# Kernel tuning notes

Hardware: AMD Instinct MI355X
Metric: run time of the kernel (lower is better)

## Reference

```python
import jax, jax.numpy as jnp
import numpy as np

NUM_RANGES = 700
K = 250
IN_DIM = 7      # 1 power + 3 elevation embed + 3 azimuth embed
HID = 32        # Q/K hidden dim
NUM_LAYERS = 2
SCALE = 1.0 / (HID ** 0.5)


def setup_inputs() -> dict:
    key = jax.random.key(0)
    ks = jax.random.split(key, 12)
    N = NUM_RANGES * K
    inp = {
        "power_vals": jax.random.normal(ks[0], (N, 1), dtype=jnp.float32),
        "ele_indices": jax.random.randint(ks[1], (N,), 0, 37),
        "azi_indices": jax.random.randint(ks[2], (N,), 0, 107),
        # learned parameters
        "ele_emb": jax.random.normal(ks[3], (37, 3), dtype=jnp.float32),
        "azi_emb": jax.random.normal(ks[4], (107, 3), dtype=jnp.float32),
        # per-layer Q/K/V linear params, stacked over layers
        "Wq": jax.random.normal(ks[5], (NUM_LAYERS, IN_DIM, HID), dtype=jnp.float32) * 0.2,
        "bq": jax.random.normal(ks[6], (NUM_LAYERS, HID), dtype=jnp.float32) * 0.02,
        "Wk": jax.random.normal(ks[7], (NUM_LAYERS, IN_DIM, HID), dtype=jnp.float32) * 0.2,
        "bk": jax.random.normal(ks[8], (NUM_LAYERS, HID), dtype=jnp.float32) * 0.02,
        "Wv": jax.random.normal(ks[9], (NUM_LAYERS, IN_DIM, 1), dtype=jnp.float32) * 0.2,
        "bv": jax.random.normal(ks[10], (NUM_LAYERS, 1), dtype=jnp.float32) * 0.02,
    }
    return inp


def reference(power_vals, ele_indices, azi_indices, ele_emb, azi_emb, Wq, bq, Wk, bk, Wv, bv):
    # x: [R, K, 1]
    x = power_vals.reshape(NUM_RANGES, K, -1)
    # embedding lookups: [R, K, 3]
    e = ele_emb[ele_indices.reshape(NUM_RANGES, K)].astype(jnp.float32)
    a = azi_emb[azi_indices.reshape(NUM_RANGES, K)].astype(jnp.float32)
    for i in range(NUM_LAYERS):
        h = jnp.concatenate([x, e, a], axis=-1)           # [R, K, 7]
        q = h @ Wq[i] + bq[i]                             # [R, K, 32]
        k = h @ Wk[i] + bk[i]                             # [R, K, 32]
        v = h @ Wv[i] + bv[i]                             # [R, K, 1]
        scores = jnp.einsum("rqd,rkd->rqk", q, k) * SCALE  # [R, K, K]
        probs = jax.nn.softmax(scores, axis=-1)
        x = jnp.einsum("rqk,rkd->rqd", probs, v)          # [R, K, 1]
    return x.reshape(NUM_RANGES * K, 1)
```

## Files before the change

### kernel.cpp

```cpp
#include <hip/hip_runtime.h>
#include <hip/hip_fp16.h>

#define NR 700
#define KK 250
#define HID 32

typedef unsigned int uint32;
typedef _Float16 f16x8 __attribute__((ext_vector_type(8)));
typedef float f32x4 __attribute__((ext_vector_type(4)));
typedef _Float16 hpair __attribute__((ext_vector_type(2)));

#if __has_builtin(__builtin_amdgcn_exp2f)
#define EXP2F(x) __builtin_amdgcn_exp2f(x)
#else
#define EXP2F(x) exp2f(x)
#endif

__device__ __forceinline__ uint32 packh2(float lo, float hi) {
    hpair p; p.x = (_Float16)lo; p.y = (_Float16)hi;
    return __builtin_bit_cast(uint32, p);
}
__device__ __forceinline__ f16x8 u4f16(uint4 u) { return __builtin_bit_cast(f16x8, u); }

__device__ __forceinline__ void compute_weights(
    int wt, int l,
    const float* __restrict__ Wq, const float* __restrict__ bq,
    const float* __restrict__ Wk,
    const float* __restrict__ Wv, const float* __restrict__ bv,
    float (*Msh)[7], float* wsh, float* wvsh, float SC2Q)
{
    const float* wq = Wq + l * 7 * HID;
    const float* wk = Wk + l * 7 * HID;
    if (wt < 49) {
        int c = wt / 7, cp = wt % 7;
        float s = 0.f;
        #pragma unroll 8
        for (int d = 0; d < HID; ++d) s = fmaf(wq[c * HID + d], wk[cp * HID + d], s);
        Msh[c][cp] = s * SC2Q;
    } else if (wt < 56) {
        int cp = wt - 49;
        float s = 0.f;
        #pragma unroll 8
        for (int d = 0; d < HID; ++d) s = fmaf(bq[l * HID + d], wk[cp * HID + d], s);
        wsh[cp] = s * SC2Q;
    } else if (wt < 63) {
        wvsh[wt - 56] = Wv[l * 7 + (wt - 56)];
    } else if (wt == 63) {
        wvsh[7] = bv[l];
    }
}

__global__ __launch_bounds__(512, 6) void mlra_kernel(
    const float* __restrict__ power,
    const int*   __restrict__ ele_idx,
    const int*   __restrict__ azi_idx,
    const float* __restrict__ ele_emb,
    const float* __restrict__ azi_emb,
    const float* __restrict__ Wq,
    const float* __restrict__ bq,
    const float* __restrict__ Wk,
    const float* __restrict__ bk,
    const float* __restrict__ Wv,
    const float* __restrict__ bv,
    float* __restrict__ out)
{
    __shared__ uint4 hh[256];
    __shared__ uint4 tt[256];
    __shared__ float vsh[256];
    __shared__ float Msh[2][7][7];
    __shared__ float wsh[2][7];
    __shared__ float wvsh[2][8];

    const int r    = blockIdx.x;
    const int tid  = threadIdx.x;
    const int lane = tid & 63;
    const int wid  = tid >> 6;
    const int col  = lane & 15;
    const int grp  = lane >> 4;

    const float SC2Q = 0.17677669529663687f * 1.4426950408889634f * 0.25f;

    if (tid < 256) {
        float hv[7];
        if (tid < KK) {
            int g = r * KK + tid;
            hv[0] = power[g];
            int ei = ele_idx[g];
            int ai = azi_idx[g];
            hv[1] = ele_emb[ei * 3 + 0];
            hv[2] = ele_emb[ei * 3 + 1];
            hv[3] = ele_emb[ei * 3 + 2];
            hv[4] = azi_emb[ai * 3 + 0];
            hv[5] = azi_emb[ai * 3 + 1];
            hv[6] = azi_emb[ai * 3 + 2];
        } else {
            #pragma unroll
            for (int c = 0; c < 7; ++c) hv[c] = 0.f;
        }
        uint4 u;
        u.x = packh2(hv[0], hv[1]);
        u.y = packh2(hv[2], hv[3]);
        u.z = packh2(hv[4], hv[5]);
        u.w = packh2(hv[6], 0.f);
        hh[tid] = u;
        vsh[tid] = 0.f;
    } else if (tid < 384) {
        int l = (tid - 256) >> 6;
        compute_weights(tid & 63, l, Wq, bq, Wk, Wv, bv, Msh[l], wsh[l], wvsh[l], SC2Q);
    }
    __syncthreads();

    const int n0 = 2 * wid;
    const int n1 = 2 * wid + 1;
    const f32x4 cz = {0.f, 0.f, 0.f, 0.f};

    float x0 = 0.f, x1 = 0.f;

    for (int l = 0; l < 2; ++l) {
        if (tid < 256) {
            uint4 u = hh[tid];
            hpair pa = __builtin_bit_cast(hpair, u.x);
            hpair pb = __builtin_bit_cast(hpair, u.y);
            hpair pc = __builtin_bit_cast(hpair, u.z);
            hpair pd = __builtin_bit_cast(hpair, u.w);
            float hv[7] = {(float)pa.x, (float)pa.y, (float)pb.x, (float)pb.y,
                           (float)pc.x, (float)pc.y, (float)pd.x};
            float tv[7];
            #pragma unroll
            for (int cp = 0; cp < 7; ++cp) {
                float s = wsh[l][cp];
                #pragma unroll
                for (int c = 0; c < 7; ++c) s = fmaf(hv[c], Msh[l][c][cp], s);
                tv[cp] = s;
            }
            float v = wvsh[l][7];
            #pragma unroll
            for (int c = 0; c < 7; ++c) v = fmaf(hv[c], wvsh[l][c], v);
            uint4 t4;
            t4.x = packh2(tv[0], tv[1]);
            t4.y = packh2(tv[2], tv[3]);
            t4.z = packh2(tv[4], tv[5]);
            t4.w = packh2(tv[6], 0.f);
            tt[tid] = t4;
            vsh[tid] = (tid < KK) ? v : 0.f;
        }
        __syncthreads();

        f16x8 bt0 = u4f16(tt[n0 * 16 + col]);
        f16x8 bt1 = u4f16(tt[n1 * 16 + col]);

        float ss0 = 0.f, oo0 = 0.f, ss1 = 0.f, oo1 = 0.f;
        #pragma unroll 2
        for (int jt = 0; jt < 16; ++jt) {
            f16x8 ah = u4f16(hh[jt * 16 + col]);
            f32x4 vv = *reinterpret_cast<const f32x4*>(&vsh[jt * 16 + grp * 4]);
            f32x4 c0 = __builtin_amdgcn_mfma_f32_16x16x32_f16(ah, bt0, cz, 0, 0, 0);
            f32x4 c1 = __builtin_amdgcn_mfma_f32_16x16x32_f16(ah, bt1, cz, 0, 0, 0);
            #pragma unroll
            for (int rg = 0; rg < 4; ++rg) {
                float p0 = EXP2F(c0[rg]);
                float p1 = EXP2F(c1[rg]);
                float vj = vv[rg];
                ss0 += p0; oo0 = fmaf(p0, vj, oo0);
                ss1 += p1; oo1 = fmaf(p1, vj, oo1);
            }
        }
        {
            int ex = 4 * grp - 6;
            ex = ex < 0 ? 0 : (ex > 4 ? 4 : ex);
            float exf = (float)ex;
            ss0 -= exf; ss1 -= exf;
        }

        ss0 += __shfl_xor(ss0, 16); ss0 += __shfl_xor(ss0, 32);
        oo0 += __shfl_xor(oo0, 16); oo0 += __shfl_xor(oo0, 32);
        ss1 += __shfl_xor(ss1, 16); ss1 += __shfl_xor(ss1, 32);
        oo1 += __shfl_xor(oo1, 16); oo1 += __shfl_xor(oo1, 32);
        x0 = oo0 / ss0;
        x1 = oo1 / ss1;

        if (l == 0) {
            __syncthreads();
            if (grp == 0) {
                int i0 = n0 * 16 + col;
                int i1 = n1 * 16 + col;
                reinterpret_cast<_Float16*>(hh)[i0 * 8] = (_Float16)x0;
                if (i1 < KK) reinterpret_cast<_Float16*>(hh)[i1 * 8] = (_Float16)x1;
            }
            __syncthreads();
        }
    }

    if (grp == 0) {
        int i0 = n0 * 16 + col;
        int i1 = n1 * 16 + col;
        out[r * KK + i0] = x0;
        if (i1 < KK) out[r * KK + i1] = x1;
    }
}

extern "C" void kernel_launch(void* const* d_in, const int* in_sizes, int n_in,
                              void* d_out, int out_size, void* d_ws, size_t ws_size,
                              hipStream_t stream) {
    const float* power   = (const float*)d_in[0];
    const int*   ele     = (const int*)d_in[1];
    const int*   azi     = (const int*)d_in[2];
    const float* ele_emb = (const float*)d_in[3];
    const float* azi_emb = (const float*)d_in[4];
    const float* Wq      = (const float*)d_in[5];
    const float* bq      = (const float*)d_in[6];
    const float* Wk      = (const float*)d_in[7];
    const float* bk      = (const float*)d_in[8];
    const float* Wv      = (const float*)d_in[9];
    const float* bv      = (const float*)d_in[10];
    float* outp = (float*)d_out;
    (void)bk;

    hipLaunchKernelGGL(mlra_kernel, dim3(NR), dim3(512), 0, stream,
                       power, ele, azi, ele_emb, azi_emb, Wq, bq, Wk, bk, Wv, bv, outp);
}
```

Baseline: 24.89 us.

## Halve block size, give each wave four query tiles, pack V in fp16

Blocks shrink from 512 to 256 threads, so each of the 4 waves now owns four 16-query column tiles instead of two. Each loop step loads two key tiles and issues eight MFMAs, which reuses every loaded A fragment across four B tiles. The V values are stored in LDS as a packed fp16 layout, so one uint4 read covers a lane's values for two key tiles. The goal is fewer LDS reads per MFMA and more work per wave, at the cost of higher register pressure, lower V precision and fewer waves per block.

```diff
diff --git a/kernel.cpp b/kernel.cpp
--- a/kernel.cpp
+++ b/kernel.cpp
@@ -50,7 +50,7 @@
     }
 }
 
-__global__ __launch_bounds__(512, 6) void mlra_kernel(
+__global__ __launch_bounds__(256, 4) void mlra_kernel(
     const float* __restrict__ power,
     const int*   __restrict__ ele_idx,
     const int*   __restrict__ azi_idx,
@@ -66,7 +66,7 @@
 {
     __shared__ uint4 hh[256];
     __shared__ uint4 tt[256];
-    __shared__ float vsh[256];
+    __shared__ uint4 vpk[8][4];
     __shared__ float Msh[2][7][7];
     __shared__ float wsh[2][7];
     __shared__ float wvsh[2][8];
@@ -80,7 +80,7 @@
 
     const float SC2Q = 0.17677669529663687f * 1.4426950408889634f * 0.25f;
 
-    if (tid < 256) {
+    {
         float hv[7];
         if (tid < KK) {
             int g = r * KK + tid;
@@ -103,21 +103,18 @@
         u.z = packh2(hv[4], hv[5]);
         u.w = packh2(hv[6], 0.f);
         hh[tid] = u;
-        vsh[tid] = 0.f;
-    } else if (tid < 384) {
-        int l = (tid - 256) >> 6;
-        compute_weights(tid & 63, l, Wq, bq, Wk, Wv, bv, Msh[l], wsh[l], wvsh[l], SC2Q);
+    }
+    if (tid < 128) {
+        compute_weights(tid & 63, tid >> 6, Wq, bq, Wk, Wv, bv,
+                        Msh[tid >> 6], wsh[tid >> 6], wvsh[tid >> 6], SC2Q);
     }
     __syncthreads();
 
-    const int n0 = 2 * wid;
-    const int n1 = 2 * wid + 1;
     const f32x4 cz = {0.f, 0.f, 0.f, 0.f};
-
-    float x0 = 0.f, x1 = 0.f;
+    float x0 = 0.f, x1 = 0.f, x2 = 0.f, x3 = 0.f;
 
     for (int l = 0; l < 2; ++l) {
-        if (tid < 256) {
+        {
             uint4 u = hh[tid];
             hpair pa = __builtin_bit_cast(hpair, u.x);
             hpair pb = __builtin_bit_cast(hpair, u.y);
@@ -142,60 +139,103 @@
             t4.z = packh2(tv[4], tv[5]);
             t4.w = packh2(tv[6], 0.f);
             tt[tid] = t4;
-            vsh[tid] = (tid < KK) ? v : 0.f;
+            int jtp = tid >> 5, halfsel = (tid >> 4) & 1, grow = (tid >> 2) & 3, rg = tid & 3;
+            reinterpret_cast<_Float16*>(vpk)[(jtp * 4 + grow) * 8 + halfsel * 4 + rg] =
+                (_Float16)((tid < KK) ? v : 0.f);
         }
         __syncthreads();
 
-        f16x8 bt0 = u4f16(tt[n0 * 16 + col]);
-        f16x8 bt1 = u4f16(tt[n1 * 16 + col]);
+        f16x8 bt0 = u4f16(tt[(wid * 4 + 0) * 16 + col]);
+        f16x8 bt1 = u4f16(tt[(wid * 4 + 1) * 16 + col]);
+        f16x8 bt2 = u4f16(tt[(wid * 4 + 2) * 16 + col]);
+        f16x8 bt3 = u4f16(tt[(wid * 4 + 3) * 16 + col]);
 
         float ss0 = 0.f, oo0 = 0.f, ss1 = 0.f, oo1 = 0.f;
-        #pragma unroll 2
-        for (int jt = 0; jt < 16; ++jt) {
-            f16x8 ah = u4f16(hh[jt * 16 + col]);
-            f32x4 vv = *reinterpret_cast<const f32x4*>(&vsh[jt * 16 + grp * 4]);
-            f32x4 c0 = __builtin_amdgcn_mfma_f32_16x16x32_f16(ah, bt0, cz, 0, 0, 0);
-            f32x4 c1 = __builtin_amdgcn_mfma_f32_16x16x32_f16(ah, bt1, cz, 0, 0, 0);
-            #pragma unroll
-            for (int rg = 0; rg < 4; ++rg) {
-                float p0 = EXP2F(c0[rg]);
-                float p1 = EXP2F(c1[rg]);
-                float vj = vv[rg];
-                ss0 += p0; oo0 = fmaf(p0, vj, oo0);
-                ss1 += p1; oo1 = fmaf(p1, vj, oo1);
+        float ss2 = 0.f, oo2 = 0.f, ss3 = 0.f, oo3 = 0.f;
+        #pragma unroll 1
+        for (int jtp = 0; jtp < 8; ++jtp) {
+            f16x8 ahe = u4f16(hh[jtp * 32 + col]);
+            f16x8 aho = u4f16(hh[jtp * 32 + 16 + col]);
+            uint4 vq  = vpk[jtp][grp];
+            hpair v01e = __builtin_bit_cast(hpair, vq.x);
+            hpair v23e = __builtin_bit_cast(hpair, vq.y);
+            hpair v01o = __builtin_bit_cast(hpair, vq.z);
+            hpair v23o = __builtin_bit_cast(hpair, vq.w);
+            float ve0 = (float)v01e.x, ve1 = (float)v01e.y;
+            float ve2 = (float)v23e.x, ve3 = (float)v23e.y;
+            float vo0 = (float)v01o.x, vo1 = (float)v01o.y;
+            float vo2 = (float)v23o.x, vo3 = (float)v23o.y;
+
+            f32x4 ce0 = __builtin_amdgcn_mfma_f32_16x16x32_f16(ahe, bt0, cz, 0, 0, 0);
+            f32x4 ce1 = __builtin_amdgcn_mfma_f32_16x16x32_f16(ahe, bt1, cz, 0, 0, 0);
+            f32x4 ce2 = __builtin_amdgcn_mfma_f32_16x16x32_f16(ahe, bt2, cz, 0, 0, 0);
+            f32x4 ce3 = __builtin_amdgcn_mfma_f32_16x16x32_f16(ahe, bt3, cz, 0, 0, 0);
+            f32x4 co0 = __builtin_amdgcn_mfma_f32_16x16x32_f16(aho, bt0, cz, 0, 0, 0);
+            f32x4 co1 = __builtin_amdgcn_mfma_f32_16x16x32_f16(aho, bt1, cz, 0, 0, 0);
+            f32x4 co2 = __builtin_amdgcn_mfma_f32_16x16x32_f16(aho, bt2, cz, 0, 0, 0);
+            f32x4 co3 = __builtin_amdgcn_mfma_f32_16x16x32_f16(aho, bt3, cz, 0, 0, 0);
+
+            #define ACC(ct, vv0, vv1, vv2, vv3, SS, OO)                         \
+            {                                                                    \
+                float p0 = EXP2F(ct[0]); float p1 = EXP2F(ct[1]);                \
+                float p2 = EXP2F(ct[2]); float p3 = EXP2F(ct[3]);                \
+                SS += (p0 + p1) + (p2 + p3);                                     \
+                OO = fmaf(p0, vv0, OO); OO = fmaf(p1, vv1, OO);                  \
+                OO = fmaf(p2, vv2, OO); OO = fmaf(p3, vv3, OO);                  \
             }
+            ACC(ce0, ve0, ve1, ve2, ve3, ss0, oo0)
+            ACC(ce1, ve0, ve1, ve2, ve3, ss1, oo1)
+            ACC(ce2, ve0, ve1, ve2, ve3, ss2, oo2)
+            ACC(ce3, ve0, ve1, ve2, ve3, ss3, oo3)
+            ACC(co0, vo0, vo1, vo2, vo3, ss0, oo0)
+            ACC(co1, vo0, vo1, vo2, vo3, ss1, oo1)
+            ACC(co2, vo0, vo1, vo2, vo3, ss2, oo2)
+            ACC(co3, vo0, vo1, vo2, vo3, ss3, oo3)
+            #undef ACC
         }
         {
             int ex = 4 * grp - 6;
             ex = ex < 0 ? 0 : (ex > 4 ? 4 : ex);
             float exf = (float)ex;
-            ss0 -= exf; ss1 -= exf;
+            ss0 -= exf; ss1 -= exf; ss2 -= exf; ss3 -= exf;
         }
 
         ss0 += __shfl_xor(ss0, 16); ss0 += __shfl_xor(ss0, 32);
         oo0 += __shfl_xor(oo0, 16); oo0 += __shfl_xor(oo0, 32);
         ss1 += __shfl_xor(ss1, 16); ss1 += __shfl_xor(ss1, 32);
         oo1 += __shfl_xor(oo1, 16); oo1 += __shfl_xor(oo1, 32);
-        x0 = oo0 / ss0;
-        x1 = oo1 / ss1;
+        ss2 += __shfl_xor(ss2, 16); ss2 += __shfl_xor(ss2, 32);
+        oo2 += __shfl_xor(oo2, 16); oo2 += __shfl_xor(oo2, 32);
+        ss3 += __shfl_xor(ss3, 16); ss3 += __shfl_xor(ss3, 32);
+        oo3 += __shfl_xor(oo3, 16); oo3 += __shfl_xor(oo3, 32);
+        x0 = oo0 / ss0; x1 = oo1 / ss1; x2 = oo2 / ss2; x3 = oo3 / ss3;
 
         if (l == 0) {
             __syncthreads();
             if (grp == 0) {
-                int i0 = n0 * 16 + col;
-                int i1 = n1 * 16 + col;
-                reinterpret_cast<_Float16*>(hh)[i0 * 8] = (_Float16)x0;
-                if (i1 < KK) reinterpret_cast<_Float16*>(hh)[i1 * 8] = (_Float16)x1;
+                int i0 = (wid * 4 + 0) * 16 + col;
+                int i1 = (wid * 4 + 1) * 16 + col;
+                int i2 = (wid * 4 + 2) * 16 + col;
+                int i3 = (wid * 4 + 3) * 16 + col;
+                _Float16* hhf = reinterpret_cast<_Float16*>(hh);
+                hhf[i0 * 8] = (_Float16)x0;
+                hhf[i1 * 8] = (_Float16)x1;
+                hhf[i2 * 8] = (_Float16)x2;
+                if (i3 < KK) hhf[i3 * 8] = (_Float16)x3;
             }
             __syncthreads();
         }
     }
 
     if (grp == 0) {
-        int i0 = n0 * 16 + col;
-        int i1 = n1 * 16 + col;
+        int i0 = (wid * 4 + 0) * 16 + col;
+        int i1 = (wid * 4 + 1) * 16 + col;
+        int i2 = (wid * 4 + 2) * 16 + col;
+        int i3 = (wid * 4 + 3) * 16 + col;
         out[r * KK + i0] = x0;
-        if (i1 < KK) out[r * KK + i1] = x1;
+        out[r * KK + i1] = x1;
+        out[r * KK + i2] = x2;
+        if (i3 < KK) out[r * KK + i3] = x3;
     }
 }
 
@@ -216,6 +256,6 @@
     float* outp = (float*)d_out;
     (void)bk;
 
-    hipLaunchKernelGGL(mlra_kernel, dim3(NR), dim3(512), 0, stream,
+    hipLaunchKernelGGL(mlra_kernel, dim3(NR), dim3(256), 0, stream,
                        power, ele, azi, ele_emb, azi_emb, Wq, bq, Wk, bk, Wv, bv, outp);
 }
```

New measurement: 23.37 us (median of 2 runs). 6.1% less time.
